# Performance work log

Measured on AMD Instinct MI355X. Metric: run time of the kernel, lower is better.

Reference implementation:

```python
import jax, jax.numpy as jnp
import numpy as np
from jax import lax

SIGMA = 4
TOPK = 9
GRID = 28          # patch grid hardcoded in AnomalyMapGenerator
IMG = 224          # input_size
SCALE = IMG // GRID  # nearest-neighbor upsample factor = 8
KSIZE = 2 * int(4.0 * SIGMA + 0.5) + 1  # 33, as in compute_anomaly_map


def _gaussian_kernel1d():
    x = jnp.arange(KSIZE, dtype=jnp.float32) - KSIZE // 2
    g = jnp.exp(-(x * x) / (2.0 * SIGMA * SIGMA))
    return g / jnp.sum(g)


def _gaussian_blur2d(x):
    # x: [B,1,H,W]; separable gaussian with reflect padding (kornia default)
    g = _gaussian_kernel1d()
    pad = KSIZE // 2
    # blur along H
    xh = jnp.pad(x, ((0, 0), (0, 0), (pad, pad), (0, 0)), mode='reflect')
    xh = lax.conv_general_dilated(xh, g.reshape(1, 1, KSIZE, 1), (1, 1), 'VALID')
    # blur along W
    xw = jnp.pad(xh, ((0, 0), (0, 0), (0, 0), (pad, pad)), mode='reflect')
    return lax.conv_general_dilated(xw, g.reshape(1, 1, 1, KSIZE), (1, 1), 'VALID')


def setup_inputs() -> dict:
    key = jax.random.key(0)
    k1, k2 = jax.random.split(key)
    embedding = jax.random.normal(k1, (3136, 1536), dtype=jnp.float32)
    memory_bank = jax.random.normal(k2, (20000, 1536), dtype=jnp.float32)  # M x D
    return {"embedding": embedding, "memory_bank": memory_bank}


def reference(embedding, memory_bank):
    x2 = jnp.sum(embedding * embedding, axis=-1, keepdims=True)        # [N,1]
    y2 = jnp.sum(memory_bank * memory_bank, axis=-1)                   # [M]
    d2 = x2 + y2[None, :] - 2.0 * (embedding @ memory_bank.T)          # [N,M]
    dist = jnp.sqrt(jnp.maximum(d2, 0.0))
    # topk smallest, ascending (matches torch.topk largest=False)
    neg_top, _ = lax.top_k(-dist, TOPK)
    patch_scores = -neg_top                                            # [N,9]

    # --- compute_anomaly_map ---
    batch = patch_scores.shape[0] // (GRID * GRID)
    amap = patch_scores[:, 0].reshape(batch, 1, GRID, GRID)
    # F.interpolate default mode='nearest' with integer factor 8 == repeat
    amap = jnp.repeat(jnp.repeat(amap, SCALE, axis=2), SCALE, axis=3)  # [B,1,224,224]
    amap = _gaussian_blur2d(amap)

    # --- compute_anomaly_score ---
    idx = jnp.argmax(patch_scores[:, 0])
    confidence = patch_scores[idx]                                     # [9]
    e = jnp.exp(confidence)
    weights = 1.0 - jnp.max(e) / jnp.sum(e)
    score = weights * jnp.max(patch_scores[:, 0])
    return amap, score
```

## Files before the change

### kernel.cpp

```cpp
#include <hip/hip_runtime.h>

typedef __attribute__((ext_vector_type(4))) int i32x4;

#define N_ROWS 3136
#define M_COLS 20000
#define KDIM   1536
#define NCT    157
#define NRT    25
#define NWG    (NCT * NRT)
#define PPR    (NCT*9)

#define QSCL   (4.0f / 127.0f)
#define QINV   (127.0f / 4.0f)
#define TWO_S2 (2.0f * QSCL * QSCL)

#define GLOAD_LDS16(g, l) __builtin_amdgcn_global_load_lds( \
    (const __attribute__((address_space(1))) unsigned int*)(g), \
    (__attribute__((address_space(3))) unsigned int*)(l), 16, 0, 0)

__device__ inline void t9_insert(float (&t)[9], float v) {
    #pragma unroll
    for (int s = 8; s >= 1; --s)
        t[s] = __builtin_amdgcn_fmed3f(v, t[s-1], t[s]);
    t[0] = fminf(t[0], v);
}

__device__ inline int q8(float x) {
    int q = (int)rintf(x * QINV);
    q = q > 127 ? 127 : q;
    q = q < -127 ? -127 : q;
    return q & 255;
}

__global__ void cvt_norm_kernel(const float* __restrict__ src,
                                unsigned char* __restrict__ dst,
                                float* __restrict__ norms, int rows) {
    int lane = threadIdx.x & 63;
    int row = blockIdx.x * (blockDim.x >> 6) + (threadIdx.x >> 6);
    if (row >= rows) return;
    const float4* p = (const float4*)(src + (size_t)row * KDIM);
    int* q = (int*)(dst + (size_t)row * KDIM);
    float s = 0.f;
    #pragma unroll
    for (int i = 0; i < 6; ++i) {
        float4 v = p[lane + i * 64];
        s += v.x*v.x + v.y*v.y + v.z*v.z + v.w*v.w;
        q[lane + i * 64] = q8(v.x) | (q8(v.y) << 8) | (q8(v.z) << 16) | (q8(v.w) << 24);
    }
    #pragma unroll
    for (int off = 32; off > 0; off >>= 1) s += __shfl_down(s, off);
    if (lane == 0) norms[row] = s;
}

union SMem {
    unsigned char stg[2][16384];
    struct { float Ds[32 * 129]; float T9[8 * 32 * 9]; } epi;
};

#define STAGE(BUF, KT) do { \
    const int koff_ = (KT) * 64; \
    GLOAD_LDS16(pa[0] + koff_, sm.stg[BUF] + ldsoff[0]); \
    GLOAD_LDS16(pa[1] + koff_, sm.stg[BUF] + ldsoff[1]); \
    GLOAD_LDS16(pb[0] + koff_, sm.stg[BUF] + 8192 + ldsoff[0]); \
    GLOAD_LDS16(pb[1] + koff_, sm.stg[BUF] + 8192 + ldsoff[1]); \
} while (0)

#define KSTEP(CB, NB, KT, PF) do { \
    if (PF) STAGE(NB, (KT) + 1); \
    i32x4 af[4], bfr[4]; \
    _Pragma("unroll") \
    for (int mi = 0; mi < 4; ++mi) \
        af[mi] = *(const i32x4*)(sm.stg[CB] + (wr + mi * 16 + l15) * 64 + kbs); \
    _Pragma("unroll") \
    for (int ni = 0; ni < 4; ++ni) \
        bfr[ni] = *(const i32x4*)(sm.stg[CB] + 8192 + (wc + ni * 16 + l15) * 64 + kbs); \
    _Pragma("unroll") \
    for (int mi = 0; mi < 4; ++mi) \
        _Pragma("unroll") \
        for (int ni = 0; ni < 4; ++ni) \
            acc[mi][ni] = __builtin_amdgcn_mfma_i32_16x16x64_i8(af[mi], bfr[ni], acc[mi][ni], 0, 0, 0); \
    asm volatile("s_waitcnt vmcnt(0)" ::: "memory"); \
    __builtin_amdgcn_s_barrier(); \
} while (0)

__global__ __launch_bounds__(256, 4) void dist_topk_kernel(
    const unsigned char* __restrict__ Aq,
    const unsigned char* __restrict__ Bq,
    const float* __restrict__ x2, const float* __restrict__ y2,
    float* __restrict__ partials)
{
    __shared__ __align__(16) SMem sm;

    const int tid = threadIdx.x;
    const int wave = tid >> 6, lane = tid & 63;

    int orig = blockIdx.x;
    int xcd = orig & 7, li = orig >> 3;
    const int qc = NWG / 8, rc = NWG % 8;
    int wg = (xcd < rc ? xcd * (qc + 1) : rc * (qc + 1) + (xcd - rc) * qc) + li;
    const int ct = wg / NRT, rt = wg % NRT;
    const int rowBase = rt * 128, colBase = ct * 128;

    const unsigned char* pa[2];
    const unsigned char* pb[2];
    int ldsoff[2];
    #pragma unroll
    for (int i = 0; i < 2; ++i) {
        int flat = i * 256 + tid;
        int r = flat >> 2;
        int kk = (((flat & 3) ^ ((flat >> 3) & 3))) * 16;
        int ar = rowBase + r; ar = ar < N_ROWS ? ar : N_ROWS - 1;
        int bc = colBase + r; bc = bc < M_COLS ? bc : M_COLS - 1;
        pa[i] = Aq + (size_t)ar * KDIM + kk;
        pb[i] = Bq + (size_t)bc * KDIM + kk;
        ldsoff[i] = flat * 16;
    }

    const int l15 = lane & 15;
    const int kb = (lane >> 4) * 16;
    const int kbs = kb ^ (((l15 >> 1) & 3) << 4);
    const int g4 = (lane >> 4) * 4;
    const int wr = (wave >> 1) * 64;
    const int wc = (wave & 1) * 64;

    i32x4 acc[4][4] = {};

    STAGE(0, 0);
    asm volatile("s_waitcnt vmcnt(0)" ::: "memory");
    __builtin_amdgcn_s_barrier();

    #pragma unroll 1
    for (int kt = 0; kt < 24; kt += 2) {
        KSTEP(0, 1, kt, 1);
        KSTEP(1, 0, kt + 1, (kt + 2) < 24);
    }

    int ncols = M_COLS - colBase; ncols = ncols < 128 ? ncols : 128;

    #pragma unroll
    for (int p = 0; p < 4; ++p) {
        __syncthreads();
        if ((wave >> 1) == (p >> 1)) {
            const int mi0 = (p & 1) * 2;
            #pragma unroll
            for (int ni = 0; ni < 4; ++ni) {
                int c = wc + ni * 16 + l15;
                int gc = colBase + c;
                float yv = y2[gc < M_COLS ? gc : M_COLS - 1];
                #pragma unroll
                for (int mh = 0; mh < 2; ++mh) {
                    #pragma unroll
                    for (int j = 0; j < 4; ++j) {
                        int rloc = mh * 16 + g4 + j;
                        int gr = rowBase + p * 32 + rloc;
                        float xv = x2[gr < N_ROWS ? gr : N_ROWS - 1];
                        sm.epi.Ds[rloc * 129 + c] = xv + yv - TWO_S2 * (float)acc[mi0 + mh][ni][j];
                    }
                }
            }
        }
        __syncthreads();
        int r = tid & 31, q8g = tid >> 5;
        int grow = rowBase + p * 32 + r;
        float t9[9];
        #pragma unroll
        for (int s = 0; s < 9; ++s) t9[s] = 3.4e38f;
        int cs = q8g * 16;
        int ce = (cs + 16 < ncols) ? cs + 16 : ncols;
        for (int c = cs; c < ce; ++c) t9_insert(t9, sm.epi.Ds[r * 129 + c]);
        #pragma unroll
        for (int s = 0; s < 9; ++s) sm.epi.T9[(q8g * 32 + r) * 9 + s] = t9[s];
        __syncthreads();
        if (q8g < 4) {
            #pragma unroll
            for (int s = 0; s < 9; ++s)
                t9_insert(t9, sm.epi.T9[((q8g + 4) * 32 + r) * 9 + s]);
            #pragma unroll
            for (int s = 0; s < 9; ++s) sm.epi.T9[(q8g * 32 + r) * 9 + s] = t9[s];
        }
        __syncthreads();
        if (q8g == 0 && grow < N_ROWS) {
            #pragma unroll
            for (int qq = 1; qq < 4; ++qq)
                #pragma unroll
                for (int s = 0; s < 9; ++s)
                    t9_insert(t9, sm.epi.T9[(qq * 32 + r) * 9 + s]);
            float* dst = partials + (size_t)grow * PPR + ct * 9;
            #pragma unroll
            for (int s = 0; s < 9; ++s) dst[s] = t9[s];
        }
    }
}

__global__ void merge_topk_kernel(const float* __restrict__ partials,
                                  float* __restrict__ scores) {
    int lane = threadIdx.x & 63;
    int row = blockIdx.x * 4 + (threadIdx.x >> 6);
    const float* p = partials + (size_t)row * PPR;
    float t9[9];
    #pragma unroll
    for (int s = 0; s < 9; ++s) t9[s] = 3.4e38f;
    for (int i = lane; i < PPR; i += 64) {
        float v = p[i];
        if (v < t9[8]) t9_insert(t9, v);
    }
    #pragma unroll
    for (int off = 32; off > 0; off >>= 1) {
        float o[9];
        #pragma unroll
        for (int s = 0; s < 9; ++s) o[s] = __shfl_xor(t9[s], off);
        #pragma unroll
        for (int s = 0; s < 9; ++s)
            if (o[s] < t9[8]) t9_insert(t9, o[s]);
    }
    if (lane == 0) {
        #pragma unroll
        for (int s = 0; s < 9; ++s)
            scores[row * 9 + s] = sqrtf(fmaxf(t9[s], 0.f));
    }
}

__global__ void blur_h_kernel(const float* __restrict__ scores, float* __restrict__ tH) {
    int idx = blockIdx.x * blockDim.x + threadIdx.x;
    if (idx >= 4 * 224 * 28) return;
    int pw = idx % 28, y = (idx / 28) % 224, b = idx / (28 * 224);
    float acc = 0.f, gsum = 0.f;
    #pragma unroll
    for (int k = 0; k < 33; ++k) {
        float xk = (float)(k - 16);
        float w = expf(-xk * xk * (1.0f / 32.0f));
        gsum += w;
        int yy = y - 16 + k;
        yy = yy < 0 ? -yy : yy;
        yy = yy > 223 ? 446 - yy : yy;
        acc += w * scores[(size_t)(b * 784 + (yy >> 3) * 28 + pw) * 9];
    }
    tH[idx] = acc / gsum;
}

__global__ void blur_w_kernel(const float* __restrict__ tH, float* __restrict__ out) {
    int idx = blockIdx.x * blockDim.x + threadIdx.x;
    if (idx >= 4 * 224 * 224) return;
    int x = idx % 224, y = (idx / 224) % 224, b = idx / (224 * 224);
    float acc = 0.f, gsum = 0.f;
    #pragma unroll
    for (int k = 0; k < 33; ++k) {
        float xk = (float)(k - 16);
        float w = expf(-xk * xk * (1.0f / 32.0f));
        gsum += w;
        int xx = x - 16 + k;
        xx = xx < 0 ? -xx : xx;
        xx = xx > 223 ? 446 - xx : xx;
        acc += w * tH[(b * 224 + y) * 28 + (xx >> 3)];
    }
    out[idx] = acc / gsum;
}

__global__ void score_kernel(const float* __restrict__ scores, float* __restrict__ out) {
    __shared__ float vmax[256];
    __shared__ int   vidx[256];
    int tid = threadIdx.x;
    float best = -3.4e38f; int bi = 0x7fffffff;
    for (int r = tid; r < N_ROWS; r += 256) {
        float v = scores[r * 9];
        if (v > best) { best = v; bi = r; }
    }
    vmax[tid] = best; vidx[tid] = bi;
    __syncthreads();
    for (int s = 128; s > 0; s >>= 1) {
        if (tid < s) {
            if (vmax[tid + s] > vmax[tid] ||
                (vmax[tid + s] == vmax[tid] && vidx[tid + s] < vidx[tid])) {
                vmax[tid] = vmax[tid + s]; vidx[tid] = vidx[tid + s];
            }
        }
        __syncthreads();
    }
    if (tid == 0) {
        int idx = vidx[0];
        float es = 0.f, em = -3.4e38f;
        #pragma unroll
        for (int s = 0; s < 9; ++s) {
            float e = expf(scores[idx * 9 + s]);
            es += e; em = fmaxf(em, e);
        }
        out[4 * 224 * 224] = (1.0f - em / es) * vmax[0];
    }
}

extern "C" void kernel_launch(void* const* d_in, const int* in_sizes, int n_in,
                              void* d_out, int out_size, void* d_ws, size_t ws_size,
                              hipStream_t stream) {
    const float* emb = (const float*)d_in[0];
    const float* mb  = (const float*)d_in[1];
    float* out = (float*)d_out;
    char* ws = (char*)d_ws;

    unsigned char* mbq      = (unsigned char*)(ws);
    unsigned char* embq     = (unsigned char*)(ws + 30720000);
    float*         x2       = (float*)(ws + 35536896);
    float*         y2       = (float*)(ws + 35549440);
    float*         partials = (float*)(ws + 35629440);
    float*         scores   = (float*)(ws + 53354112);
    float*         tH       = (float*)(ws + 53467008);

    cvt_norm_kernel<<<M_COLS / 4, 256, 0, stream>>>(mb, mbq, y2, M_COLS);
    cvt_norm_kernel<<<N_ROWS / 4, 256, 0, stream>>>(emb, embq, x2, N_ROWS);
    dist_topk_kernel<<<NWG, 256, 0, stream>>>(embq, mbq, x2, y2, partials);
    merge_topk_kernel<<<N_ROWS / 4, 256, 0, stream>>>(partials, scores);
    blur_h_kernel<<<(4 * 224 * 28 + 255) / 256, 256, 0, stream>>>(scores, tH);
    blur_w_kernel<<<(4 * 224 * 224 + 255) / 256, 256, 0, stream>>>(tH, out);
    score_kernel<<<1, 256, 0, stream>>>(scores, out);
}
```

Before: 209.8 us.

## Split int8 GEMM tile across 8 waves with smaller per-wave accumulators

The distance-topk kernel now launches 512 threads per workgroup instead of 256. Each of the 8 waves computes a 64x32 sub-tile, so there are 8 accumulators per wave instead of 16, and each thread issues one async global-to-LDS load per operand instead of two. The MFMA loop is also reordered to interleave fragment loads with MFMAs, keeping register pressure low enough for higher occupancy (launch bounds 512,8). The epilogue top-k stays on the first 256 threads, leaving half the threads idle there and adding barrier cost with the larger workgroup.

```diff
diff --git a/kernel.cpp b/kernel.cpp
--- a/kernel.cpp
+++ b/kernel.cpp
@@ -59,31 +59,33 @@
 
 #define STAGE(BUF, KT) do { \
     const int koff_ = (KT) * 64; \
-    GLOAD_LDS16(pa[0] + koff_, sm.stg[BUF] + ldsoff[0]); \
-    GLOAD_LDS16(pa[1] + koff_, sm.stg[BUF] + ldsoff[1]); \
-    GLOAD_LDS16(pb[0] + koff_, sm.stg[BUF] + 8192 + ldsoff[0]); \
-    GLOAD_LDS16(pb[1] + koff_, sm.stg[BUF] + 8192 + ldsoff[1]); \
+    GLOAD_LDS16(pa + koff_, sm.stg[BUF] + ldsoff); \
+    GLOAD_LDS16(pb + koff_, sm.stg[BUF] + 8192 + ldsoff); \
 } while (0)
+
+#define MFMA_I8 __builtin_amdgcn_mfma_i32_16x16x64_i8
 
 #define KSTEP(CB, NB, KT, PF) do { \
     if (PF) STAGE(NB, (KT) + 1); \
-    i32x4 af[4], bfr[4]; \
-    _Pragma("unroll") \
-    for (int mi = 0; mi < 4; ++mi) \
-        af[mi] = *(const i32x4*)(sm.stg[CB] + (wr + mi * 16 + l15) * 64 + kbs); \
-    _Pragma("unroll") \
-    for (int ni = 0; ni < 4; ++ni) \
-        bfr[ni] = *(const i32x4*)(sm.stg[CB] + 8192 + (wc + ni * 16 + l15) * 64 + kbs); \
-    _Pragma("unroll") \
-    for (int mi = 0; mi < 4; ++mi) \
-        _Pragma("unroll") \
-        for (int ni = 0; ni < 4; ++ni) \
-            acc[mi][ni] = __builtin_amdgcn_mfma_i32_16x16x64_i8(af[mi], bfr[ni], acc[mi][ni], 0, 0, 0); \
+    i32x4 bf0 = *(const i32x4*)(sm.stg[CB] + 8192 + (wc +  0 + l15) * 64 + kbs); \
+    i32x4 bf1 = *(const i32x4*)(sm.stg[CB] + 8192 + (wc + 16 + l15) * 64 + kbs); \
+    i32x4 af0 = *(const i32x4*)(sm.stg[CB] + (wr +  0 + l15) * 64 + kbs); \
+    i32x4 af1 = *(const i32x4*)(sm.stg[CB] + (wr + 16 + l15) * 64 + kbs); \
+    acc[0][0] = MFMA_I8(af0, bf0, acc[0][0], 0, 0, 0); \
+    acc[0][1] = MFMA_I8(af0, bf1, acc[0][1], 0, 0, 0); \
+    acc[1][0] = MFMA_I8(af1, bf0, acc[1][0], 0, 0, 0); \
+    acc[1][1] = MFMA_I8(af1, bf1, acc[1][1], 0, 0, 0); \
+    af0 = *(const i32x4*)(sm.stg[CB] + (wr + 32 + l15) * 64 + kbs); \
+    af1 = *(const i32x4*)(sm.stg[CB] + (wr + 48 + l15) * 64 + kbs); \
+    acc[2][0] = MFMA_I8(af0, bf0, acc[2][0], 0, 0, 0); \
+    acc[2][1] = MFMA_I8(af0, bf1, acc[2][1], 0, 0, 0); \
+    acc[3][0] = MFMA_I8(af1, bf0, acc[3][0], 0, 0, 0); \
+    acc[3][1] = MFMA_I8(af1, bf1, acc[3][1], 0, 0, 0); \
     asm volatile("s_waitcnt vmcnt(0)" ::: "memory"); \
     __builtin_amdgcn_s_barrier(); \
 } while (0)
 
-__global__ __launch_bounds__(256, 4) void dist_topk_kernel(
+__global__ __launch_bounds__(512, 8) void dist_topk_kernel(
     const unsigned char* __restrict__ Aq,
     const unsigned char* __restrict__ Bq,
     const float* __restrict__ x2, const float* __restrict__ y2,
@@ -92,7 +94,8 @@
     __shared__ __align__(16) SMem sm;
 
     const int tid = threadIdx.x;
-    const int wave = tid >> 6, lane = tid & 63;
+    const int wid = tid >> 6, lane = tid & 63;
+    const int wm = wid >> 2, wn = wid & 3;
 
     int orig = blockIdx.x;
     int xcd = orig & 7, li = orig >> 3;
@@ -101,29 +104,27 @@
     const int ct = wg / NRT, rt = wg % NRT;
     const int rowBase = rt * 128, colBase = ct * 128;
 
-    const unsigned char* pa[2];
-    const unsigned char* pb[2];
-    int ldsoff[2];
-    #pragma unroll
-    for (int i = 0; i < 2; ++i) {
-        int flat = i * 256 + tid;
-        int r = flat >> 2;
-        int kk = (((flat & 3) ^ ((flat >> 3) & 3))) * 16;
+    const unsigned char* pa;
+    const unsigned char* pb;
+    int ldsoff;
+    {
+        int r = tid >> 2;
+        int kk = ((tid & 3) ^ ((tid >> 3) & 3)) * 16;
         int ar = rowBase + r; ar = ar < N_ROWS ? ar : N_ROWS - 1;
         int bc = colBase + r; bc = bc < M_COLS ? bc : M_COLS - 1;
-        pa[i] = Aq + (size_t)ar * KDIM + kk;
-        pb[i] = Bq + (size_t)bc * KDIM + kk;
-        ldsoff[i] = flat * 16;
+        pa = Aq + (size_t)ar * KDIM + kk;
+        pb = Bq + (size_t)bc * KDIM + kk;
+        ldsoff = tid * 16;
     }
 
     const int l15 = lane & 15;
     const int kb = (lane >> 4) * 16;
     const int kbs = kb ^ (((l15 >> 1) & 3) << 4);
     const int g4 = (lane >> 4) * 4;
-    const int wr = (wave >> 1) * 64;
-    const int wc = (wave & 1) * 64;
-
-    i32x4 acc[4][4] = {};
+    const int wr = wm * 64;
+    const int wc = wn * 32;
+
+    i32x4 acc[4][2] = {};
 
     STAGE(0, 0);
     asm volatile("s_waitcnt vmcnt(0)" ::: "memory");
@@ -140,10 +141,10 @@
     #pragma unroll
     for (int p = 0; p < 4; ++p) {
         __syncthreads();
-        if ((wave >> 1) == (p >> 1)) {
+        if (wm == (p >> 1)) {
             const int mi0 = (p & 1) * 2;
             #pragma unroll
-            for (int ni = 0; ni < 4; ++ni) {
+            for (int ni = 0; ni < 2; ++ni) {
                 int c = wc + ni * 16 + l15;
                 int gc = colBase + c;
                 float yv = y2[gc < M_COLS ? gc : M_COLS - 1];
@@ -161,17 +162,18 @@
         }
         __syncthreads();
         int r = tid & 31, q8g = tid >> 5;
-        int grow = rowBase + p * 32 + r;
         float t9[9];
         #pragma unroll
         for (int s = 0; s < 9; ++s) t9[s] = 3.4e38f;
-        int cs = q8g * 16;
-        int ce = (cs + 16 < ncols) ? cs + 16 : ncols;
-        for (int c = cs; c < ce; ++c) t9_insert(t9, sm.epi.Ds[r * 129 + c]);
-        #pragma unroll
-        for (int s = 0; s < 9; ++s) sm.epi.T9[(q8g * 32 + r) * 9 + s] = t9[s];
-        __syncthreads();
-        if (q8g < 4) {
+        if (tid < 256) {
+            int cs = q8g * 16;
+            int ce = (cs + 16 < ncols) ? cs + 16 : ncols;
+            for (int c = cs; c < ce; ++c) t9_insert(t9, sm.epi.Ds[r * 129 + c]);
+            #pragma unroll
+            for (int s = 0; s < 9; ++s) sm.epi.T9[(q8g * 32 + r) * 9 + s] = t9[s];
+        }
+        __syncthreads();
+        if (tid < 256 && q8g < 4) {
             #pragma unroll
             for (int s = 0; s < 9; ++s)
                 t9_insert(t9, sm.epi.T9[((q8g + 4) * 32 + r) * 9 + s]);
@@ -179,7 +181,8 @@
             for (int s = 0; s < 9; ++s) sm.epi.T9[(q8g * 32 + r) * 9 + s] = t9[s];
         }
         __syncthreads();
-        if (q8g == 0 && grow < N_ROWS) {
+        int grow = rowBase + p * 32 + r;
+        if (tid < 256 && q8g == 0 && grow < N_ROWS) {
             #pragma unroll
             for (int qq = 1; qq < 4; ++qq)
                 #pragma unroll
@@ -306,7 +309,7 @@
 
     cvt_norm_kernel<<<M_COLS / 4, 256, 0, stream>>>(mb, mbq, y2, M_COLS);
     cvt_norm_kernel<<<N_ROWS / 4, 256, 0, stream>>>(emb, embq, x2, N_ROWS);
-    dist_topk_kernel<<<NWG, 256, 0, stream>>>(embq, mbq, x2, y2, partials);
+    dist_topk_kernel<<<NWG, 512, 0, stream>>>(embq, mbq, x2, y2, partials);
     merge_topk_kernel<<<N_ROWS / 4, 256, 0, stream>>>(partials, scores);
     blur_h_kernel<<<(4 * 224 * 28 + 255) / 256, 256, 0, stream>>>(scores, tH);
     blur_w_kernel<<<(4 * 224 * 224 + 255) / 256, 256, 0, stream>>>(tH, out);
```

Measured after the change: 223.1 us. 1.06x slower.
